# Kernel tuning notes

Measured on AMD Instinct MI355X. Metric: run time of the kernel, lower is better.

## Reference

```python
import jax, jax.numpy as jnp
import numpy as np

D_MODEL = 1024
N_HEAD = 16
D_FF = 4096
B, S = 2, 2048


def _layernorm(x, g, b, eps=1e-5):
    mu = jnp.mean(x, axis=-1, keepdims=True)
    var = jnp.var(x, axis=-1, keepdims=True)
    return (x - mu) * jax.lax.rsqrt(var + eps) * g + b


def setup_inputs() -> dict:
    key = jax.random.key(0)
    ks = jax.random.split(key, 12)
    s = 0.02
    return {
        "x": jax.random.normal(ks[0], (B, S, D_MODEL), dtype=jnp.float32),
        "src_mask": jnp.zeros((B, 1, 1, S), dtype=jnp.float32),
        "w_q": jax.random.normal(ks[1], (D_MODEL, D_MODEL), dtype=jnp.float32) * s,
        "b_q": jnp.zeros((D_MODEL,), dtype=jnp.float32),
        "w_k": jax.random.normal(ks[2], (D_MODEL, D_MODEL), dtype=jnp.float32) * s,
        "b_k": jnp.zeros((D_MODEL,), dtype=jnp.float32),
        "w_v": jax.random.normal(ks[3], (D_MODEL, D_MODEL), dtype=jnp.float32) * s,
        "b_v": jnp.zeros((D_MODEL,), dtype=jnp.float32),
        "w_o": jax.random.normal(ks[4], (D_MODEL, D_MODEL), dtype=jnp.float32) * s,
        "b_o": jnp.zeros((D_MODEL,), dtype=jnp.float32),
        "w_ff1": jax.random.normal(ks[5], (D_MODEL, D_FF), dtype=jnp.float32) * s,
        "b_ff1": jnp.zeros((D_FF,), dtype=jnp.float32),
        "w_ff2": jax.random.normal(ks[6], (D_FF, D_MODEL), dtype=jnp.float32) * s,
        "b_ff2": jnp.zeros((D_MODEL,), dtype=jnp.float32),
        "ln1_g": jnp.ones((D_MODEL,), dtype=jnp.float32),
        "ln1_b": jnp.zeros((D_MODEL,), dtype=jnp.float32),
        "ln2_g": jnp.ones((D_MODEL,), dtype=jnp.float32),
        "ln2_b": jnp.zeros((D_MODEL,), dtype=jnp.float32),
    }


def reference(x, src_mask, w_q, b_q, w_k, b_k, w_v, b_v, w_o, b_o,
              w_ff1, b_ff1, w_ff2, b_ff2, ln1_g, ln1_b, ln2_g, ln2_b):
    b, s, d = x.shape
    dh = d // N_HEAD

    def split(t):  # [b,s,d] -> [b,h,s,dh]
        return t.reshape(b, s, N_HEAD, dh).transpose(0, 2, 1, 3)

    q = split(x @ w_q + b_q)
    k = split(x @ w_k + b_k)
    v = split(x @ w_v + b_v)

    # naive full-score attention, as in the source module
    score = jnp.einsum('bhqd,bhkd->bhqk', q, k) / jnp.sqrt(jnp.float32(dh))
    score = score + src_mask
    attn = jax.nn.softmax(score, axis=-1)
    out = jnp.einsum('bhqk,bhkd->bhqd', attn, v)
    out = out.transpose(0, 2, 1, 3).reshape(b, s, d)
    out = out @ w_o + b_o

    x = _layernorm(x + out, ln1_g, ln1_b)

    ff = jax.nn.relu(x @ w_ff1 + b_ff1) @ w_ff2 + b_ff2
    x = _layernorm(x + ff, ln2_g, ln2_b)
    return x
```

## Files before the change

kernel.cpp:

```cpp
#include <hip/hip_runtime.h>
#include <cstdint>
#include <cstddef>

#define BATCH 2
#define SEQ 2048
#define DMODEL 1024
#define NHEAD 16
#define DFF 4096
#define MTOT (BATCH * SEQ)

typedef __bf16 bf16x8 __attribute__((ext_vector_type(8)));
typedef __bf16 bf16x4 __attribute__((ext_vector_type(4)));
typedef short s16x4 __attribute__((ext_vector_type(4)));
typedef float f32x4 __attribute__((ext_vector_type(4)));

#define S_BARRIER() __builtin_amdgcn_s_barrier()
#define SCHED_FENCE() __builtin_amdgcn_sched_barrier(0)
#define VMCNT8() asm volatile("s_waitcnt vmcnt(8)" ::: "memory")
#define VMCNT4() asm volatile("s_waitcnt vmcnt(4)" ::: "memory")
#define VMCNT0() asm volatile("s_waitcnt vmcnt(0)" ::: "memory")

__device__ __forceinline__ void gload_lds16(const void* g, void* l) {
  __builtin_amdgcn_global_load_lds(
      (__attribute__((address_space(1))) void*)(uintptr_t)g,
      (__attribute__((address_space(3))) void*)(uint32_t)(uintptr_t)l,
      16, 0, 0);
}

__global__ __launch_bounds__(256) void k_prep(
    const float* __restrict__ wq, const float* __restrict__ wk,
    const float* __restrict__ wv, const float* __restrict__ wo,
    const float* __restrict__ wff1, const float* __restrict__ wff2,
    __bf16* __restrict__ wqkvT, __bf16* __restrict__ woT,
    __bf16* __restrict__ wff1T, __bf16* __restrict__ wff2T,
    const float* __restrict__ bq, const float* __restrict__ bk,
    const float* __restrict__ bv, float* __restrict__ bqkv,
    const float* __restrict__ mask, float* __restrict__ mask2,
    const float* __restrict__ x, __bf16* __restrict__ xbf) {
  int f = blockIdx.x;
  if (f < 12) {
    const int i = f * 256 + threadIdx.x;
    if (i < 3072)
      bqkv[i] = (i < 1024) ? bq[i] : (i < 2048) ? bk[i - 1024] : bv[i - 2048];
    return;
  }
  f -= 12;
  if (f < 16) {
    const int i = f * 256 + threadIdx.x;
    if (i < BATCH * SEQ) mask2[i] = mask[i] * 1.44269504f;
    return;
  }
  f -= 16;
  if (f < 4096) {
    const int i = (f * 256 + threadIdx.x) * 4;
    const float4 v = *(const float4*)(x + i);
    bf16x4 r;
    r[0] = (__bf16)v.x; r[1] = (__bf16)v.y; r[2] = (__bf16)v.z; r[3] = (__bf16)v.w;
    *(bf16x4*)(xbf + i) = r;
    return;
  }
  f -= 4096;
  const float* src;
  __bf16* dst;
  int Kd, Nd, n0, k0;
  if (f < 3072) {
    const int zz = f / 1024, r = f % 1024;
    src = (zz == 0) ? wq : (zz == 1) ? wk : wv;
    dst = wqkvT + (size_t)zz * 1024 * 1024;
    Kd = 1024; Nd = 1024; n0 = (r & 31) * 32; k0 = (r >> 5) * 32;
  } else if (f < 4096) {
    const int r = f - 3072;
    src = wo; dst = woT;
    Kd = 1024; Nd = 1024; n0 = (r & 31) * 32; k0 = (r >> 5) * 32;
  } else if (f < 8192) {
    const int r = f - 4096;
    src = wff1; dst = wff1T;
    Kd = 1024; Nd = 4096; n0 = (r & 127) * 32; k0 = (r >> 7) * 32;
  } else {
    const int r = f - 8192;
    src = wff2; dst = wff2T;
    Kd = 4096; Nd = 1024; n0 = (r & 31) * 32; k0 = (r >> 5) * 32;
  }
  __shared__ float t[32][33];
  const int tx = threadIdx.x & 31, ty = threadIdx.x >> 5;
#pragma unroll
  for (int i = ty; i < 32; i += 8) t[i][tx] = src[(size_t)(k0 + i) * Nd + n0 + tx];
  __syncthreads();
#pragma unroll
  for (int i = ty; i < 32; i += 8)
    dst[(size_t)(n0 + i) * Kd + k0 + tx] = (__bf16)t[tx][i];
}

__global__ __launch_bounds__(256) void k_transpose_v(
    const __bf16* __restrict__ qkvb, __bf16* __restrict__ vT) {
  __shared__ __bf16 t[32][33];
  const int s0 = blockIdx.x * 32, c0 = blockIdx.y * 32, b = blockIdx.z;
  const int tx = threadIdx.x & 31, ty = threadIdx.x >> 5;
#pragma unroll
  for (int i = ty; i < 32; i += 8)
    t[i][tx] = qkvb[(size_t)(b * SEQ + s0 + i) * 3072 + 2048 + c0 + tx];
  __syncthreads();
#pragma unroll
  for (int i = ty; i < 32; i += 8)
    vT[((size_t)b * 1024 + c0 + i) * SEQ + s0 + tx] = t[tx][i];
}

template <bool RELU, typename OutT>
__global__ __launch_bounds__(512) void k_gemm256(
    const __bf16* __restrict__ A, const __bf16* __restrict__ BT,
    const float* __restrict__ bias, OutT* __restrict__ C,
    int M, int N, int K) {
  __shared__ __align__(16) __bf16 sA[4 * 8192];
  __shared__ __align__(16) __bf16 sB[4 * 8192];
  const int tid = threadIdx.x, lane = tid & 63, wv = tid >> 6;
  const int wm = wv >> 2, wn = wv & 3;
  const int lrow = lane & 15, hi = lane >> 4;
  const int nwg = gridDim.x * gridDim.y;
  const int flat = blockIdx.y * gridDim.x + blockIdx.x;
  const int cpx = nwg >> 3;
  const int swzb = (flat & 7) * cpx + (flat >> 3);
  const int m0 = (swzb / gridDim.x) * 256;
  const int n0 = (swzb % gridDim.x) * 256;
  const int NT = K >> 6;

  const int lsub = lane >> 2;
  const int gg = (lane & 3) ^ ((lane >> 3) & 3);
  const int gr = hi ^ ((lrow >> 1) & 3);

  f32x4 acc[8][4];
#pragma unroll
  for (int r = 0; r < 8; ++r)
#pragma unroll
    for (int c = 0; c < 4; ++c) acc[r][c] = f32x4{0.f, 0.f, 0.f, 0.f};

  auto stage = [&](int p) {
    const int tile = p >> 1;
    const int slot = (((tile & 1) * 2) + (p & 1)) * 8192;
    const int kcol = tile * 64 + (p & 1) * 32 + gg * 8;
#pragma unroll
    for (int i = 0; i < 2; ++i) {
      const int c = wv * 2 + i;
      gload_lds16(A + (size_t)(m0 + c * 16 + lsub) * K + kcol, &sA[slot + c * 512]);
      gload_lds16(BT + (size_t)(n0 + c * 16 + lsub) * K + kcol, &sB[slot + c * 512]);
    }
  };

  auto compute = [&](int p) {
    const int slot = ((((p >> 1) & 1) * 2) + (p & 1)) * 8192;
    bf16x8 af[8], bfv[4];
#pragma unroll
    for (int r = 0; r < 8; ++r)
      af[r] = *(const bf16x8*)&sA[slot + (wm * 128 + r * 16 + lrow) * 32 + gr * 8];
#pragma unroll
    for (int c = 0; c < 4; ++c)
      bfv[c] = *(const bf16x8*)&sB[slot + (wn * 64 + c * 16 + lrow) * 32 + gr * 8];
    __builtin_amdgcn_s_setprio(1);
#pragma unroll
    for (int r = 0; r < 8; ++r)
#pragma unroll
      for (int c = 0; c < 4; ++c)
        acc[r][c] = __builtin_amdgcn_mfma_f32_16x16x32_bf16(af[r], bfv[c],
                                                            acc[r][c], 0, 0, 0);
    __builtin_amdgcn_s_setprio(0);
  };

  stage(0); stage(1); stage(2);
  int p = 0;
  for (; p < 2 * NT - 3; ++p) {
    VMCNT8(); S_BARRIER(); SCHED_FENCE();
    stage(p + 3);
    compute(p);
  }
  VMCNT8(); S_BARRIER(); SCHED_FENCE(); compute(p); ++p;
  VMCNT4(); S_BARRIER(); SCHED_FENCE(); compute(p); ++p;
  VMCNT0(); S_BARRIER(); SCHED_FENCE(); compute(p);

#pragma unroll
  for (int r = 0; r < 8; ++r) {
    const int row = m0 + wm * 128 + r * 16 + hi * 4;
#pragma unroll
    for (int c = 0; c < 4; ++c) {
      const int col = n0 + wn * 64 + c * 16 + lrow;
      const float bb = bias[col];
#pragma unroll
      for (int j = 0; j < 4; ++j) {
        float v = acc[r][c][j] + bb;
        if (RELU) v = fmaxf(v, 0.f);
        C[(size_t)(row + j) * N + col] = (OutT)v;
      }
    }
  }
}

template <int MF, bool RELU, typename OutT>
__global__ __launch_bounds__(256) void k_gemm(
    const __bf16* __restrict__ A, const __bf16* __restrict__ BT,
    const float* __restrict__ bias, OutT* __restrict__ C0,
    OutT* __restrict__ C1, int M, int N, int lda, int KS) {
  __shared__ __bf16 sA[MF * 32 * 64];
  __shared__ __bf16 sB[128 * 64];
  const int tid = threadIdx.x, lane = tid & 63, wv = tid >> 6;
  const int wm = wv >> 1, wn = wv & 1;
  const int lrow = lane & 15, hi = lane >> 4;
  const int nwg = gridDim.x * gridDim.y;
  const int flat = blockIdx.y * gridDim.x + blockIdx.x;
  const int cpx = nwg >> 3;
  const int swzb = (flat & 7) * cpx + (flat >> 3);
  const int m0 = (swzb / gridDim.x) * (MF * 32);
  const int n0 = (swzb % gridDim.x) * 128;
  const int koff = blockIdx.z * KS;
  OutT* Cz = blockIdx.z ? C1 : C0;
  const int srow = lane >> 3;
  const int scolE = ((lane & 7) ^ srow) * 8;
  const int swz = (lrow & 7) << 4;

  f32x4 acc[MF][4];
#pragma unroll
  for (int r = 0; r < MF; ++r)
#pragma unroll
    for (int c = 0; c < 4; ++c) acc[r][c] = f32x4{0.f, 0.f, 0.f, 0.f};

  for (int k0 = 0; k0 < KS; k0 += 64) {
    __syncthreads();
#pragma unroll
    for (int rb = wv; rb < MF * 4; rb += 4) {
      const int row = rb * 8 + srow;
      gload_lds16(A + (size_t)(m0 + row) * lda + koff + k0 + scolE, &sA[rb * 512]);
    }
#pragma unroll
    for (int rb = wv; rb < 16; rb += 4) {
      const int row = rb * 8 + srow;
      gload_lds16(BT + (size_t)(n0 + row) * lda + koff + k0 + scolE, &sB[rb * 512]);
    }
    __syncthreads();
#pragma unroll
    for (int kc = 0; kc < 2; ++kc) {
      bf16x8 af[MF], bfr[4];
#pragma unroll
      for (int r = 0; r < MF; ++r) {
        const int row = wm * (MF * 16) + r * 16 + lrow;
        af[r] = *(const bf16x8*)((const char*)sA + row * 128 + ((kc * 64 + hi * 16) ^ swz));
      }
#pragma unroll
      for (int c = 0; c < 4; ++c) {
        const int row = wn * 64 + c * 16 + lrow;
        bfr[c] = *(const bf16x8*)((const char*)sB + row * 128 + ((kc * 64 + hi * 16) ^ swz));
      }
#pragma unroll
      for (int r = 0; r < MF; ++r)
#pragma unroll
        for (int c = 0; c < 4; ++c)
          acc[r][c] = __builtin_amdgcn_mfma_f32_16x16x32_bf16(af[r], bfr[c],
                                                              acc[r][c], 0, 0, 0);
    }
  }

#pragma unroll
  for (int r = 0; r < MF; ++r) {
    const int row = m0 + wm * (MF * 16) + r * 16 + hi * 4;
#pragma unroll
    for (int c = 0; c < 4; ++c) {
      const int col = n0 + wn * 64 + c * 16 + lrow;
      const float bb = (blockIdx.z == 0) ? bias[col] : 0.f;
#pragma unroll
      for (int j = 0; j < 4; ++j) {
        float v = acc[r][c][j] + bb;
        if (RELU) v = fmaxf(v, 0.f);
        Cz[(size_t)(row + j) * N + col] = (OutT)v;
      }
    }
  }
}

__global__ __launch_bounds__(512) void k_attn(
    const __bf16* __restrict__ qkv, const __bf16* __restrict__ vT,
    const float* __restrict__ mask2, __bf16* __restrict__ out) {
  const int nwg = gridDim.x * gridDim.y * gridDim.z;
  const int flat = (blockIdx.z * gridDim.y + blockIdx.y) * gridDim.x + blockIdx.x;
  const int cpx = nwg >> 3;
  const int swzb = (flat & 7) * cpx + (flat >> 3);
  const int qb = swzb & (gridDim.x - 1);
  const int h = (swzb >> 4) & 15;
  const int b = swzb >> 8;
  const int tid = threadIdx.x, lane = tid & 63, wv = tid >> 6;
  const int lrow = lane & 15, hi = lane >> 4;

  __shared__ __bf16 sK[2][128 * 64];
  __shared__ __bf16 sV0[2][64 * 64];
  __shared__ __bf16 sV1[2][64 * 64];

  const size_t base = (size_t)b * SEQ * 3072;
  const __bf16* Qb = qkv + base + h * 64;
  const __bf16* Kb = qkv + base + 1024 + h * 64;
  const __bf16* vTb = vT + ((size_t)b * 1024 + h * 64) * SEQ;
  const float* maskb = mask2 + (size_t)b * SEQ;

  const int q0 = qb * 128 + wv * 16;
  const bf16x8 qf0 = *(const bf16x8*)&Qb[(size_t)(q0 + lrow) * 3072 + hi * 8];
  const bf16x8 qf1 = *(const bf16x8*)&Qb[(size_t)(q0 + lrow) * 3072 + 32 + hi * 8];

  float m_r = -3e38f, l_r = 0.f;
  f32x4 o[4];
#pragma unroll
  for (int d = 0; d < 4; ++d) o[d] = f32x4{0.f, 0.f, 0.f, 0.f};

  const int srow = lane >> 3;
  const int scolE = ((lane & 7) ^ srow) * 8;
  const int swz = (lrow & 7) << 4;

  auto stage = [&](int t) {
    const int k0s = t * 128;
    __bf16* dK = sK[t & 1];
    __bf16* dV0 = sV0[t & 1];
    __bf16* dV1 = sV1[t & 1];
#pragma unroll
    for (int r = 0; r < 2; ++r) {
      const int rb = wv + r * 8;
      const int row = rb * 8 + srow;
      gload_lds16(Kb + (size_t)(k0s + row) * 3072 + scolE, &dK[rb * 512]);
    }
    const int vrow = wv * 8 + srow;
    gload_lds16(vTb + (size_t)vrow * SEQ + k0s + scolE, &dV0[wv * 512]);
    gload_lds16(vTb + (size_t)vrow * SEQ + k0s + 64 + scolE, &dV1[wv * 512]);
  };

  stage(0);
  const int NT = SEQ / 128;
  for (int t = 0; t < NT; ++t) {
    __syncthreads();
    if (t + 1 < NT) stage(t + 1);
    const __bf16* cK = sK[t & 1];
    const __bf16* cV0 = sV0[t & 1];
    const __bf16* cV1 = sV1[t & 1];
    const int k0 = t * 128;

    f32x4 st[8];
#pragma unroll
    for (int t4 = 0; t4 < 8; ++t4) {
      const char* rp = (const char*)cK + (t4 * 16 + lrow) * 128;
      const bf16x8 ka = *(const bf16x8*)(rp + ((hi * 16) ^ swz));
      const bf16x8 kb = *(const bf16x8*)(rp + ((64 + hi * 16) ^ swz));
      f32x4 a = f32x4{0.f, 0.f, 0.f, 0.f};
      a = __builtin_amdgcn_mfma_f32_16x16x32_bf16(ka, qf0, a, 0, 0, 0);
      a = __builtin_amdgcn_mfma_f32_16x16x32_bf16(kb, qf1, a, 0, 0, 0);
      st[t4] = a;
    }

    float pm = -3e38f;
#pragma unroll
    for (int t4 = 0; t4 < 8; ++t4) {
      const f32x4 mk = *(const f32x4*)&maskb[k0 + t4 * 16 + hi * 4];
#pragma unroll
      for (int j = 0; j < 4; ++j) {
        st[t4][j] = st[t4][j] * 0.18033688f + mk[j];
        pm = fmaxf(pm, st[t4][j]);
      }
    }
    pm = fmaxf(pm, __shfl_xor(pm, 16));
    pm = fmaxf(pm, __shfl_xor(pm, 32));

    if (__any(pm > m_r + 11.5f)) {
      const float mn = fmaxf(m_r, pm);
      const float so = __builtin_amdgcn_exp2f(m_r - mn);
      m_r = mn;
      l_r *= so;
      float so_o[4];
#pragma unroll
      for (int jj = 0; jj < 4; ++jj) so_o[jj] = __shfl(so, hi * 4 + jj);
#pragma unroll
      for (int d = 0; d < 4; ++d)
#pragma unroll
        for (int jj = 0; jj < 4; ++jj) o[d][jj] *= so_o[jj];
    }

    float rs = 0.f;
#pragma unroll
    for (int t4 = 0; t4 < 8; ++t4)
#pragma unroll
      for (int j = 0; j < 4; ++j) {
        st[t4][j] = __builtin_amdgcn_exp2f(st[t4][j] - m_r);
        rs += st[t4][j];
      }
    rs += __shfl_xor(rs, 16);
    rs += __shfl_xor(rs, 32);
    l_r += rs;

    s16x4 pa[8];
#pragma unroll
    for (int t4 = 0; t4 < 8; ++t4)
#pragma unroll
      for (int j = 0; j < 4; ++j) {
        const __bf16 pb = (__bf16)st[t4][j];
        pa[t4][j] = __builtin_bit_cast(short, pb);
      }

#pragma unroll
    for (int d = 0; d < 4; ++d) {
      const char* rp0 = (const char*)cV0 + (d * 16 + lrow) * 128;
      const char* rp1 = (const char*)cV1 + (d * 16 + lrow) * 128;
#pragma unroll
      for (int t4 = 0; t4 < 4; ++t4) {
        const s16x4 vb0 = *(const s16x4*)(rp0 + ((t4 * 32 + hi * 8) ^ swz));
        o[d] = __builtin_amdgcn_mfma_f32_16x16x16bf16_1k(pa[t4], vb0, o[d], 0, 0, 0);
        const s16x4 vb1 = *(const s16x4*)(rp1 + ((t4 * 32 + hi * 8) ^ swz));
        o[d] = __builtin_amdgcn_mfma_f32_16x16x16bf16_1k(pa[4 + t4], vb1, o[d], 0, 0, 0);
      }
    }
  }

  __syncthreads();
  float linv[4];
#pragma unroll
  for (int jj = 0; jj < 4; ++jj) linv[jj] = 1.0f / __shfl(l_r, hi * 4 + jj);
#pragma unroll
  for (int d = 0; d < 4; ++d)
#pragma unroll
    for (int jj = 0; jj < 4; ++jj)
      out[((size_t)b * SEQ + q0 + hi * 4 + jj) * DMODEL + h * 64 + d * 16 + lrow] =
          (__bf16)(o[d][jj] * linv[jj]);
}

__global__ __launch_bounds__(256) void k_add_ln(
    const float* __restrict__ x, const float* __restrict__ y,
    const float* __restrict__ y2, const float* __restrict__ g,
    const float* __restrict__ be, float* __restrict__ of,
    __bf16* __restrict__ ob) {
  const int row = blockIdx.x, tid = threadIdx.x;
  const float4 a = ((const float4*)(x + (size_t)row * 1024))[tid];
  float4 b = {0.f, 0.f, 0.f, 0.f};
  if (y) b = ((const float4*)(y + (size_t)row * 1024))[tid];
  float4 c = {0.f, 0.f, 0.f, 0.f};
  if (y2) c = ((const float4*)(y2 + (size_t)row * 1024))[tid];
  const float v0 = a.x + b.x + c.x, v1 = a.y + b.y + c.y;
  const float v2 = a.z + b.z + c.z, v3 = a.w + b.w + c.w;
  float s = v0 + v1 + v2 + v3;
  float s2 = v0 * v0 + v1 * v1 + v2 * v2 + v3 * v3;
#pragma unroll
  for (int off = 32; off > 0; off >>= 1) {
    s += __shfl_xor(s, off);
    s2 += __shfl_xor(s2, off);
  }
  __shared__ float red[2][4];
  const int wv = tid >> 6, lane = tid & 63;
  if (lane == 0) { red[0][wv] = s; red[1][wv] = s2; }
  __syncthreads();
  s = red[0][0] + red[0][1] + red[0][2] + red[0][3];
  s2 = red[1][0] + red[1][1] + red[1][2] + red[1][3];
  const float mean = s * (1.0f / 1024.0f);
  const float var = s2 * (1.0f / 1024.0f) - mean * mean;
  const float rstd = rsqrtf(var + 1e-5f);
  const float4 gg = ((const float4*)g)[tid];
  const float4 bt = ((const float4*)be)[tid];
  float4 r;
  r.x = (v0 - mean) * rstd * gg.x + bt.x;
  r.y = (v1 - mean) * rstd * gg.y + bt.y;
  r.z = (v2 - mean) * rstd * gg.z + bt.z;
  r.w = (v3 - mean) * rstd * gg.w + bt.w;
  ((float4*)(of + (size_t)row * 1024))[tid] = r;
  if (ob) {
    bf16x4 rb;
    rb[0] = (__bf16)r.x; rb[1] = (__bf16)r.y; rb[2] = (__bf16)r.z; rb[3] = (__bf16)r.w;
    *(bf16x4*)(ob + (size_t)row * 1024 + tid * 4) = rb;
  }
}

extern "C" void kernel_launch(void* const* d_in, const int* in_sizes, int n_in,
                              void* d_out, int out_size, void* d_ws, size_t ws_size,
                              hipStream_t stream) {
  const float* x = (const float*)d_in[0];
  const float* src_mask = (const float*)d_in[1];
  const float* w_q = (const float*)d_in[2];
  const float* b_q = (const float*)d_in[3];
  const float* w_k = (const float*)d_in[4];
  const float* b_k = (const float*)d_in[5];
  const float* w_v = (const float*)d_in[6];
  const float* b_v = (const float*)d_in[7];
  const float* w_o = (const float*)d_in[8];
  const float* b_o = (const float*)d_in[9];
  const float* w_ff1 = (const float*)d_in[10];
  const float* b_ff1 = (const float*)d_in[11];
  const float* w_ff2 = (const float*)d_in[12];
  const float* b_ff2 = (const float*)d_in[13];
  const float* ln1_g = (const float*)d_in[14];
  const float* ln1_b = (const float*)d_in[15];
  const float* ln2_g = (const float*)d_in[16];
  const float* ln2_b = (const float*)d_in[17];

  char* ws = (char*)d_ws;
  constexpr size_t O_WQKVT = 0;
  constexpr size_t O_WOT = O_WQKVT + 3072ull * 1024 * 2;
  constexpr size_t O_WFF1T = O_WOT + 1024ull * 1024 * 2;
  constexpr size_t O_WFF2T = O_WFF1T + 4096ull * 1024 * 2;
  constexpr size_t O_BQKV = O_WFF2T + 4096ull * 1024 * 2;
  constexpr size_t O_XBF = O_BQKV + 3072ull * 4;
  constexpr size_t O_QKV = O_XBF + 4096ull * 1024 * 2;
  constexpr size_t O_ATTN = O_QKV + 4096ull * 3072 * 2;
  constexpr size_t O_PROJ = O_ATTN + 4096ull * 1024 * 2;
  constexpr size_t O_H1F = O_PROJ + 4096ull * 1024 * 4;
  constexpr size_t O_H1B = O_H1F + 4096ull * 1024 * 4;
  constexpr size_t O_MASK2 = O_H1B + 4096ull * 1024 * 2;
  constexpr size_t O_VT = O_PROJ;
  constexpr size_t O_FF = O_QKV;
  constexpr size_t O_FF2A = O_PROJ;
  constexpr size_t O_FF2B = 0;

  __bf16* wqkvT = (__bf16*)(ws + O_WQKVT);
  __bf16* woT = (__bf16*)(ws + O_WOT);
  __bf16* wff1T = (__bf16*)(ws + O_WFF1T);
  __bf16* wff2T = (__bf16*)(ws + O_WFF2T);
  float* bqkv = (float*)(ws + O_BQKV);
  __bf16* xbf = (__bf16*)(ws + O_XBF);
  __bf16* qkvb = (__bf16*)(ws + O_QKV);
  __bf16* attnb = (__bf16*)(ws + O_ATTN);
  float* proj = (float*)(ws + O_PROJ);
  float* h1f = (float*)(ws + O_H1F);
  __bf16* h1b = (__bf16*)(ws + O_H1B);
  float* mask2 = (float*)(ws + O_MASK2);
  __bf16* vT = (__bf16*)(ws + O_VT);
  __bf16* ffb = (__bf16*)(ws + O_FF);
  float* ff2a = (float*)(ws + O_FF2A);
  float* ff2b = (float*)(ws + O_FF2B);

  k_prep<<<16412, 256, 0, stream>>>(w_q, w_k, w_v, w_o, w_ff1, w_ff2,
                                    wqkvT, woT, wff1T, wff2T,
                                    b_q, b_k, b_v, bqkv,
                                    src_mask, mask2, x, xbf);

  k_gemm256<false, __bf16><<<dim3(12, 16), 512, 0, stream>>>(xbf, wqkvT, bqkv, qkvb,
                                                             MTOT, 3072, 1024);
  k_transpose_v<<<dim3(64, 32, 2), 256, 0, stream>>>(qkvb, vT);
  k_attn<<<dim3(SEQ / 128, NHEAD, BATCH), 512, 0, stream>>>(qkvb, vT, mask2, attnb);
  k_gemm<2, false, float><<<dim3(8, 64, 1), 256, 0, stream>>>(
      attnb, woT, b_o, proj, nullptr, MTOT, 1024, 1024, 1024);
  k_add_ln<<<4096, 256, 0, stream>>>(x, proj, nullptr, ln1_g, ln1_b, h1f, h1b);
  k_gemm256<true, __bf16><<<dim3(16, 16), 512, 0, stream>>>(h1b, wff1T, b_ff1, ffb,
                                                            MTOT, DFF, 1024);
  k_gemm<2, false, float><<<dim3(8, 64, 2), 256, 0, stream>>>(
      ffb, wff2T, b_ff2, ff2a, ff2b, MTOT, 1024, DFF, 2048);
  k_add_ln<<<4096, 256, 0, stream>>>(ff2a, h1f, ff2b, ln2_g, ln2_b,
                                     (float*)d_out, nullptr);
}
```

Before: 243.3 us.

## Store GEMM outputs and residual intermediates in bf16 and vectorize V transpose

The out-projection and FF2 split-K partial outputs are now written as bf16 instead of fp32. The first layernorm no longer writes an fp32 copy of its output, and the second layernorm takes its residual from the bf16 h1 buffer. This roughly halves the intermediate traffic between the GEMMs and the layernorm kernels. The V transpose kernel is also rewritten to use 64x64 tiles with 16-byte vector loads and stores. The cost is lower precision in the residual path and in the split-K partial sums, which could affect accuracy.

```diff
diff --git a/kernel.cpp b/kernel.cpp
--- a/kernel.cpp
+++ b/kernel.cpp
@@ -25,6 +25,14 @@
       (__attribute__((address_space(1))) void*)(uintptr_t)g,
       (__attribute__((address_space(3))) void*)(uint32_t)(uintptr_t)l,
       16, 0, 0);
+}
+
+__device__ __forceinline__ float4 load4(const float* p, size_t idx) {
+  return ((const float4*)p)[idx];
+}
+__device__ __forceinline__ float4 load4(const __bf16* p, size_t idx) {
+  const bf16x4 v = ((const bf16x4*)p)[idx];
+  return float4{(float)v[0], (float)v[1], (float)v[2], (float)v[3]};
 }
 
 __global__ __launch_bounds__(256) void k_prep(
@@ -93,16 +101,25 @@
 
 __global__ __launch_bounds__(256) void k_transpose_v(
     const __bf16* __restrict__ qkvb, __bf16* __restrict__ vT) {
-  __shared__ __bf16 t[32][33];
-  const int s0 = blockIdx.x * 32, c0 = blockIdx.y * 32, b = blockIdx.z;
-  const int tx = threadIdx.x & 31, ty = threadIdx.x >> 5;
-#pragma unroll
-  for (int i = ty; i < 32; i += 8)
-    t[i][tx] = qkvb[(size_t)(b * SEQ + s0 + i) * 3072 + 2048 + c0 + tx];
+  __shared__ __bf16 t[64][72];
+  const int s0 = blockIdx.x * 64, c0 = blockIdx.y * 64, b = blockIdx.z;
+  const int vc = threadIdx.x & 7;
+  const int rw = threadIdx.x >> 3;
+#pragma unroll
+  for (int half = 0; half < 2; ++half) {
+    const int row = rw + half * 32;
+    *(bf16x8*)&t[row][vc * 8] =
+        *(const bf16x8*)&qkvb[(size_t)(b * SEQ + s0 + row) * 3072 + 2048 + c0 + vc * 8];
+  }
   __syncthreads();
 #pragma unroll
-  for (int i = ty; i < 32; i += 8)
-    vT[((size_t)b * 1024 + c0 + i) * SEQ + s0 + tx] = t[tx][i];
+  for (int half = 0; half < 2; ++half) {
+    const int c = rw + half * 32;
+    bf16x8 v;
+#pragma unroll
+    for (int i = 0; i < 8; ++i) v[i] = t[vc * 8 + i][c];
+    *(bf16x8*)&vT[((size_t)b * 1024 + c0 + c) * SEQ + s0 + vc * 8] = v;
+  }
 }
 
 template <bool RELU, typename OutT>
@@ -420,17 +437,19 @@
           (__bf16)(o[d][jj] * linv[jj]);
 }
 
+template <typename TX, typename TY, typename TY2>
 __global__ __launch_bounds__(256) void k_add_ln(
-    const float* __restrict__ x, const float* __restrict__ y,
-    const float* __restrict__ y2, const float* __restrict__ g,
+    const TX* __restrict__ x, const TY* __restrict__ y,
+    const TY2* __restrict__ y2, const float* __restrict__ g,
     const float* __restrict__ be, float* __restrict__ of,
     __bf16* __restrict__ ob) {
   const int row = blockIdx.x, tid = threadIdx.x;
-  const float4 a = ((const float4*)(x + (size_t)row * 1024))[tid];
+  const size_t idx = (size_t)row * 256 + tid;
+  const float4 a = load4(x, idx);
   float4 b = {0.f, 0.f, 0.f, 0.f};
-  if (y) b = ((const float4*)(y + (size_t)row * 1024))[tid];
+  if (y) b = load4(y, idx);
   float4 c = {0.f, 0.f, 0.f, 0.f};
-  if (y2) c = ((const float4*)(y2 + (size_t)row * 1024))[tid];
+  if (y2) c = load4(y2, idx);
   const float v0 = a.x + b.x + c.x, v1 = a.y + b.y + c.y;
   const float v2 = a.z + b.z + c.z, v3 = a.w + b.w + c.w;
   float s = v0 + v1 + v2 + v3;
@@ -456,7 +475,7 @@
   r.y = (v1 - mean) * rstd * gg.y + bt.y;
   r.z = (v2 - mean) * rstd * gg.z + bt.z;
   r.w = (v3 - mean) * rstd * gg.w + bt.w;
-  ((float4*)(of + (size_t)row * 1024))[tid] = r;
+  if (of) ((float4*)(of + (size_t)row * 1024))[tid] = r;
   if (ob) {
     bf16x4 rb;
     rb[0] = (__bf16)r.x; rb[1] = (__bf16)r.y; rb[2] = (__bf16)r.z; rb[3] = (__bf16)r.w;
@@ -501,6 +520,7 @@
   constexpr size_t O_MASK2 = O_H1B + 4096ull * 1024 * 2;
   constexpr size_t O_VT = O_PROJ;
   constexpr size_t O_FF = O_QKV;
+  constexpr size_t O_PROJB = O_PROJ;
   constexpr size_t O_FF2A = O_PROJ;
   constexpr size_t O_FF2B = 0;
 
@@ -512,14 +532,13 @@
   __bf16* xbf = (__bf16*)(ws + O_XBF);
   __bf16* qkvb = (__bf16*)(ws + O_QKV);
   __bf16* attnb = (__bf16*)(ws + O_ATTN);
-  float* proj = (float*)(ws + O_PROJ);
-  float* h1f = (float*)(ws + O_H1F);
+  __bf16* projb = (__bf16*)(ws + O_PROJB);
   __bf16* h1b = (__bf16*)(ws + O_H1B);
   float* mask2 = (float*)(ws + O_MASK2);
   __bf16* vT = (__bf16*)(ws + O_VT);
   __bf16* ffb = (__bf16*)(ws + O_FF);
-  float* ff2a = (float*)(ws + O_FF2A);
-  float* ff2b = (float*)(ws + O_FF2B);
+  __bf16* ff2a = (__bf16*)(ws + O_FF2A);
+  __bf16* ff2b = (__bf16*)(ws + O_FF2B);
 
   k_prep<<<16412, 256, 0, stream>>>(w_q, w_k, w_v, w_o, w_ff1, w_ff2,
                                     wqkvT, woT, wff1T, wff2T,
@@ -528,15 +547,16 @@
 
   k_gemm256<false, __bf16><<<dim3(12, 16), 512, 0, stream>>>(xbf, wqkvT, bqkv, qkvb,
                                                              MTOT, 3072, 1024);
-  k_transpose_v<<<dim3(64, 32, 2), 256, 0, stream>>>(qkvb, vT);
+  k_transpose_v<<<dim3(32, 16, 2), 256, 0, stream>>>(qkvb, vT);
   k_attn<<<dim3(SEQ / 128, NHEAD, BATCH), 512, 0, stream>>>(qkvb, vT, mask2, attnb);
-  k_gemm<2, false, float><<<dim3(8, 64, 1), 256, 0, stream>>>(
-      attnb, woT, b_o, proj, nullptr, MTOT, 1024, 1024, 1024);
-  k_add_ln<<<4096, 256, 0, stream>>>(x, proj, nullptr, ln1_g, ln1_b, h1f, h1b);
+  k_gemm<2, false, __bf16><<<dim3(8, 64, 1), 256, 0, stream>>>(
+      attnb, woT, b_o, projb, nullptr, MTOT, 1024, 1024, 1024);
+  k_add_ln<float, __bf16, float><<<4096, 256, 0, stream>>>(
+      x, projb, (const float*)nullptr, ln1_g, ln1_b, nullptr, h1b);
   k_gemm256<true, __bf16><<<dim3(16, 16), 512, 0, stream>>>(h1b, wff1T, b_ff1, ffb,
                                                             MTOT, DFF, 1024);
-  k_gemm<2, false, float><<<dim3(8, 64, 2), 256, 0, stream>>>(
+  k_gemm<2, false, __bf16><<<dim3(8, 64, 2), 256, 0, stream>>>(
       ffb, wff2T, b_ff2, ff2a, ff2b, MTOT, 1024, DFF, 2048);
-  k_add_ln<<<4096, 256, 0, stream>>>(ff2a, h1f, ff2b, ln2_g, ln2_b,
-                                     (float*)d_out, nullptr);
-}
+  k_add_ln<__bf16, __bf16, __bf16><<<4096, 256, 0, stream>>>(
+      ff2a, h1b, ff2b, ln2_g, ln2_b, (float*)d_out, nullptr);
+}
```

New measurement: 235.2 us. -3.3%, faster.
